# Kernel tuning notes

Measured on AMD Instinct MI355X. Metric: run time of the kernel, lower is better.

## Reference

```python
import jax, jax.numpy as jnp
import numpy as np

D_MODEL, N_HEADS, D_HEAD = 1024, 16, 64
B, T = 4, 2048


def setup_inputs() -> dict:
    key = jax.random.key(0)
    k1, k2, k3 = jax.random.split(key, 3)
    x = jax.random.normal(k1, (B, T, D_MODEL), dtype=jnp.float32)
    w_qkv = jax.random.normal(k2, (3 * N_HEADS * D_HEAD, D_MODEL), dtype=jnp.float32) * 0.02
    w_out = jax.random.normal(k3, (D_MODEL, N_HEADS * D_HEAD), dtype=jnp.float32) * 0.02
    return {"x": x, "w_qkv": w_qkv, "w_out": w_out}


def reference(x, w_qkv, w_out):
    Bx, Tx, Dx = x.shape
    scale = D_HEAD ** (-0.5)
    qkv = jnp.einsum('btd,ed->bte', x, w_qkv)  # [B,T,3*H*Dh]
    q, k, v = jnp.split(qkv, 3, axis=-1)
    def heads(t):  # [B,T,H*Dh] -> [B,H,T,Dh]
        return t.reshape(Bx, Tx, N_HEADS, D_HEAD).transpose(0, 2, 1, 3)
    q, k, v = heads(q), heads(k), heads(v)
    att = jnp.einsum('bhqd,bhkd->bhqk', q, k) * scale
    causal = jnp.tril(jnp.ones((Tx, Tx), dtype=bool))
    att = jnp.where(causal, att, -jnp.inf)
    att = jax.nn.softmax(att, axis=-1)
    y = jnp.einsum('bhqk,bhkd->bhqd', att, v)
    y = y.transpose(0, 2, 1, 3).reshape(Bx, Tx, N_HEADS * D_HEAD)
    return jnp.einsum('bte,de->btd', y, w_out)
```

## Files before the change

kernel.cpp:

```cpp
#include <hip/hip_runtime.h>
#include <hip/hip_bf16.h>

#define T_SEQ   2048
#define HEADS   16
#define DH      64
#define DMODEL  1024
#define EQKV    3072
#define BT_TOT  8192

typedef __attribute__((ext_vector_type(8)))  __bf16 bf16x8;
typedef __attribute__((ext_vector_type(4)))  float  f32x4;
typedef __attribute__((ext_vector_type(16))) float  f32x16;
typedef unsigned short ushort_t;
typedef unsigned int   uint_t;

__device__ __forceinline__ ushort_t f2bfu(float x) {
    union { float f; uint_t u; } c; c.f = x;
    uint_t u = c.u;
    uint_t r = (u + 0x7fffu + ((u >> 16) & 1u)) >> 16;
    return (ushort_t)r;
}

__device__ __forceinline__ uint_t cvtpk(float lo, float hi) {
    uint_t r;
    asm volatile("v_cvt_pk_bf16_f32 %0, %1, %2" : "=v"(r) : "v"(lo), "v"(hi));
    return r;
}

__device__ __forceinline__ void gload16(const ushort_t* g, ushort_t* l) {
    __builtin_amdgcn_global_load_lds(
        (const __attribute__((address_space(1))) void*)g,
        (__attribute__((address_space(3))) void*)l,
        16, 0, 0);
}

__global__ void cvt_f32_bf16(const float* __restrict__ in, ushort_t* __restrict__ out, int n4) {
    int i = blockIdx.x * blockDim.x + threadIdx.x;
    if (i >= n4) return;
    const float4 v = ((const float4*)in)[i];
    ushort_t r0 = f2bfu(v.x), r1 = f2bfu(v.y), r2 = f2bfu(v.z), r3 = f2bfu(v.w);
    uint_t lo = (uint_t)r0 | ((uint_t)r1 << 16);
    uint_t hi = (uint_t)r2 | ((uint_t)r3 << 16);
    ((uint2*)out)[i] = make_uint2(lo, hi);
}

#define BM 128
#define BN 128
#define BK 32

template<int MODE>
__global__ __launch_bounds__(256) void gemm_bt(const ushort_t* __restrict__ A,
                                               const ushort_t* __restrict__ Bt,
                                               void* __restrict__ Cv,
                                               ushort_t* __restrict__ VtOut,
                                               int M, int N, int K) {
    __shared__ __align__(16) ushort_t As[BM * BK];
    __shared__ __align__(16) ushort_t Bs[BN * BK];

    const int tid  = threadIdx.x;
    const int gx   = gridDim.x;
    int flat = blockIdx.y * gx + blockIdx.x;
    const int nwg  = gx * gridDim.y;
    flat = (flat & 7) * (nwg >> 3) + (flat >> 3);
    const int bn   = flat % gx, bm = flat / gx;
    const int row0 = bm * BM, col0 = bn * BN;
    const int wid  = tid >> 6, lane = tid & 63;
    const int wr   = wid >> 1, wc = wid & 1;
    const int lr   = lane & 15, lg = lane >> 4;

    const int lrow = lane >> 2;
    const int lcol = (lane & 3) * 8;

    f32x4 acc[4][4] = {};

    for (int k0 = 0; k0 < K; k0 += BK) {
        #pragma unroll
        for (int it = 0; it < 2; ++it) {
            const int c = wid * 2 + it;
            const int r = c * 16 + lrow;
            gload16(&A [(size_t)(row0 + r) * K + k0 + lcol], &As[c * 512]);
            gload16(&Bt[(size_t)(col0 + r) * K + k0 + lcol], &Bs[c * 512]);
        }
        __syncthreads();

        bf16x8 bfr[4];
        #pragma unroll
        for (int n = 0; n < 4; ++n)
            bfr[n] = *(const bf16x8*)&Bs[(wc * 64 + n * 16 + lr) * BK + lg * 8];
        #pragma unroll
        for (int m = 0; m < 4; ++m) {
            bf16x8 a = *(const bf16x8*)&As[(wr * 64 + m * 16 + lr) * BK + lg * 8];
            #pragma unroll
            for (int n = 0; n < 4; ++n)
                acc[m][n] = __builtin_amdgcn_mfma_f32_16x16x32_bf16(a, bfr[n], acc[m][n], 0, 0, 0);
        }
        __syncthreads();
    }

    if (MODE == 2 && col0 >= 2048) {
        #pragma unroll
        for (int m = 0; m < 4; ++m) {
            int rowb = row0 + wr * 64 + m * 16 + lg * 4;
            #pragma unroll
            for (int n = 0; n < 4; ++n) {
                int e = col0 - 2048 + wc * 64 + n * 16 + lr;
                uint_t lo = (uint_t)f2bfu(acc[m][n][0]) | ((uint_t)f2bfu(acc[m][n][1]) << 16);
                uint_t hi = (uint_t)f2bfu(acc[m][n][2]) | ((uint_t)f2bfu(acc[m][n][3]) << 16);
                *(uint2*)&VtOut[(size_t)e * BT_TOT + rowb] = make_uint2(lo, hi);
            }
        }
    } else {
        const int ostride = (MODE == 2) ? 2048 : N;
        #pragma unroll
        for (int m = 0; m < 4; ++m) {
            int rowb = row0 + wr * 64 + m * 16 + lg * 4;
            #pragma unroll
            for (int n = 0; n < 4; ++n) {
                int col = col0 + wc * 64 + n * 16 + lr;
                #pragma unroll
                for (int i = 0; i < 4; ++i) {
                    if (MODE == 2)
                        ((ushort_t*)Cv)[(size_t)(rowb + i) * ostride + col] = f2bfu(acc[m][n][i]);
                    else
                        ((float*)Cv)[(size_t)(rowb + i) * ostride + col] = acc[m][n][i];
                }
            }
        }
    }
}

__global__ __launch_bounds__(128, 2) void attn_fwd(const ushort_t* __restrict__ qk,
                                                   const ushort_t* __restrict__ vt,
                                                   ushort_t* __restrict__ y) {
    const int flat = blockIdx.x;
    const int xcd  = flat & 7;
    const int s    = flat >> 3;
    const int bh   = xcd * 8 + (s & 7);
    const int bx   = 31 - (s >> 3);
    const int b    = bh >> 4, h = bh & 15;
    const int tid  = threadIdx.x, lane = tid & 63;
    const int w    = tid >> 6;
    const int i    = lane & 31;
    const int hh   = lane >> 5;
    const int bT   = b * T_SEQ;

    __shared__ __align__(16) ushort_t KsL[2][64 * 64];
    __shared__ __align__(16) ushort_t VlL[2][64 * 64];

    const int q0 = bx * 64 + w * 32;
    const int qg = q0 + i;

    bf16x8 qf[4];
    {
        const ushort_t* qrow = qk + (size_t)(bT + qg) * 2048 + h * DH;
        #pragma unroll
        for (int kd = 0; kd < 4; ++kd) {
            bf16x8 q = *(const bf16x8*)&qrow[kd * 16 + hh * 8];
            #pragma unroll
            for (int j = 0; j < 8; ++j)
                ((ushort_t*)&q)[j] = f2bfu(__bfloat162float(
                    *(const __hip_bfloat16*)&((ushort_t*)&q)[j]) * 0.125f);
            qf[kd] = q;
        }
    }

    const int lr8    = lane >> 3;
    const int schunk = ((lane & 7) ^ lr8) * 8;
    const int rbase  = w * 32;

    float m = -1e30f, lsum = 0.f;
    f32x16 o0 = {}, o1 = {};

    const int nt = bx + 1;

    #pragma unroll
    for (int it = 0; it < 4; ++it) {
        const int rg = rbase + it * 8;
        const int r  = rg + lr8;
        gload16(&qk[(size_t)(bT + r) * 2048 + 1024 + h * DH + schunk], &KsL[0][rg * 64]);
        gload16(&vt[(size_t)(h * DH + r) * BT_TOT + bT + schunk],      &VlL[0][rg * 64]);
    }
    __syncthreads();

    for (int t = 0; t < nt; ++t) {
        const int cb = t & 1, nb = cb ^ 1;
        const bool has_next = (t + 1 < nt);
        const int kmin = t * 64;

        if (has_next) {
            const int kt = kmin + 64;
            #pragma unroll
            for (int it = 0; it < 4; ++it) {
                const int rg = rbase + it * 8;
                const int r  = rg + lr8;
                gload16(&qk[(size_t)(bT + kt + r) * 2048 + 1024 + h * DH + schunk], &KsL[nb][rg * 64]);
                gload16(&vt[(size_t)(h * DH + r) * BT_TOT + bT + kt + schunk],      &VlL[nb][rg * 64]);
            }
        }

        f32x16 st[2] = {};
        __builtin_amdgcn_s_setprio(1);
        #pragma unroll
        for (int kd = 0; kd < 4; ++kd) {
            const int cq = kd * 2 + hh;
            bf16x8 ka0 = *(const bf16x8*)&KsL[cb][i * 64        + ((cq ^ (i & 7)) * 8)];
            bf16x8 ka1 = *(const bf16x8*)&KsL[cb][(32 + i) * 64 + ((cq ^ (i & 7)) * 8)];
            st[0] = __builtin_amdgcn_mfma_f32_32x32x16_bf16(ka0, qf[kd], st[0], 0, 0, 0);
            st[1] = __builtin_amdgcn_mfma_f32_32x32x16_bf16(ka1, qf[kd], st[1], 0, 0, 0);
        }
        __builtin_amdgcn_s_setprio(0);

        const bool needmask = (kmin + 63) > q0;
        float pm = -1e30f;
        #pragma unroll
        for (int g = 0; g < 2; ++g) {
            #pragma unroll
            for (int r = 0; r < 16; ++r) {
                float v = st[g][r];
                if (needmask) {
                    int kv = kmin + g * 32 + (r & 3) + 8 * (r >> 2) + 4 * hh;
                    v = (kv <= qg) ? v : -1e30f;
                    st[g][r] = v;
                }
                pm = fmaxf(pm, v);
            }
        }
        pm = fmaxf(pm, __shfl_xor(pm, 32));

        if (!__all(pm - m <= 8.f)) {
            const float mnew = fmaxf(m, pm);
            const float corr = __expf(m - mnew);
            m = mnew;
            lsum *= corr;
            #pragma unroll
            for (int r = 0; r < 16; ++r) { o0[r] *= corr; o1[r] *= corr; }
        }
        float rs = 0.f;
        #pragma unroll
        for (int g = 0; g < 2; ++g) {
            #pragma unroll
            for (int r = 0; r < 16; ++r) {
                float p = __expf(st[g][r] - m);
                st[g][r] = p;
                rs += p;
            }
        }
        rs += __shfl_xor(rs, 32);
        lsum += rs;

        #pragma unroll
        for (int ks = 0; ks < 4; ++ks) {
            const int g = ks >> 1, b0 = (ks & 1) * 8;
            uint_t w0 = cvtpk(st[g][b0 + 0], st[g][b0 + 1]);
            uint_t w1 = cvtpk(st[g][b0 + 2], st[g][b0 + 3]);
            uint_t w2 = cvtpk(st[g][b0 + 4], st[g][b0 + 5]);
            uint_t w3 = cvtpk(st[g][b0 + 6], st[g][b0 + 7]);
            uint_t e0 = (uint_t)__shfl_xor((int)w0, 32);
            uint_t e1 = (uint_t)__shfl_xor((int)w1, 32);
            uint_t e2 = (uint_t)__shfl_xor((int)w2, 32);
            uint_t e3 = (uint_t)__shfl_xor((int)w3, 32);
            union { uint_t u[4]; bf16x8 v; } fr;
            fr.u[0] = hh ? e2 : w0;
            fr.u[1] = hh ? e3 : w1;
            fr.u[2] = hh ? w2 : e0;
            fr.u[3] = hh ? w3 : e1;
            const int ct = ks * 2 + hh;
            bf16x8 va0 = *(const bf16x8*)&VlL[cb][i * 64        + ((ct ^ (i & 7)) * 8)];
            bf16x8 va1 = *(const bf16x8*)&VlL[cb][(32 + i) * 64 + ((ct ^ (i & 7)) * 8)];
            __builtin_amdgcn_s_setprio(1);
            o0 = __builtin_amdgcn_mfma_f32_32x32x16_bf16(va0, fr.v, o0, 0, 0, 0);
            o1 = __builtin_amdgcn_mfma_f32_32x32x16_bf16(va1, fr.v, o1, 0, 0, 0);
            __builtin_amdgcn_s_setprio(0);
        }

        __syncthreads();
    }

    const float inv = 1.f / lsum;
    ushort_t* yrow = y + (size_t)(bT + qg) * (HEADS * DH) + h * DH;
    #pragma unroll
    for (int df = 0; df < 2; ++df) {
        const f32x16 oo = df ? o1 : o0;
        #pragma unroll
        for (int q4 = 0; q4 < 4; ++q4) {
            uint_t w0 = cvtpk(oo[q4 * 4 + 0] * inv, oo[q4 * 4 + 1] * inv);
            uint_t w1 = cvtpk(oo[q4 * 4 + 2] * inv, oo[q4 * 4 + 3] * inv);
            uint2 pk = make_uint2(w0, w1);
            *(uint2*)&yrow[df * 32 + q4 * 8 + hh * 4] = pk;
        }
    }
}

extern "C" void kernel_launch(void* const* d_in, const int* in_sizes, int n_in,
                              void* d_out, int out_size, void* d_ws, size_t ws_size,
                              hipStream_t stream) {
    const float* x     = (const float*)d_in[0];
    const float* w_qkv = (const float*)d_in[1];
    const float* w_out = (const float*)d_in[2];

    const int BT = BT_TOT;

    char* ws = (char*)d_ws;
    ushort_t* xb  = (ushort_t*)(ws);
    ushort_t* wqb = (ushort_t*)(ws + 16777216);
    ushort_t* wob = (ushort_t*)(ws + 23068672);
    ushort_t* qkb = (ushort_t*)(ws + 25165824);
    ushort_t* vtb = (ushort_t*)(ws + 58720256);
    ushort_t* yb  = (ushort_t*)(ws + 75497472);

    {
        int n4 = (BT * DMODEL) / 4;
        cvt_f32_bf16<<<(n4 + 255) / 256, 256, 0, stream>>>(x, xb, n4);
        n4 = (EQKV * DMODEL) / 4;
        cvt_f32_bf16<<<(n4 + 255) / 256, 256, 0, stream>>>(w_qkv, wqb, n4);
        n4 = (DMODEL * DMODEL) / 4;
        cvt_f32_bf16<<<(n4 + 255) / 256, 256, 0, stream>>>(w_out, wob, n4);
    }

    {
        dim3 grid(EQKV / BN, BT / BM);
        gemm_bt<2><<<grid, 256, 0, stream>>>(xb, wqb, (void*)qkb, vtb, BT, EQKV, DMODEL);
    }

    {
        attn_fwd<<<2048, 128, 0, stream>>>(qkb, vtb, yb);
    }

    {
        dim3 grid(DMODEL / BN, BT / BM);
        gemm_bt<0><<<grid, 256, 0, stream>>>(yb, wob, d_out, nullptr, BT, DMODEL, DMODEL);
    }
}
```

Baseline: 284.3 us.

## Use 128-query attention blocks with four waves, permlane swaps and exp2 softmax

Each attention block now covers 128 query rows with four waves (256 threads) that share one double-buffered K/V tile stream, which halves global K/V loads per query. Waves whose query range sits entirely before a key tile skip that tile's compute, though they still wait at the barrier. The cross-half reductions and the P-fragment exchange use permlane32_swap instead of ds shuffles. Softmax moves to base-2 by folding log2(e) into the Q scale and calling v_exp_f32 directly. In exchange, causal imbalance inside a block grows and the kernel asks for higher occupancy through launch bounds.

```diff
diff --git a/kernel.cpp b/kernel.cpp
--- a/kernel.cpp
+++ b/kernel.cpp
@@ -11,6 +11,7 @@
 typedef __attribute__((ext_vector_type(8)))  __bf16 bf16x8;
 typedef __attribute__((ext_vector_type(4)))  float  f32x4;
 typedef __attribute__((ext_vector_type(16))) float  f32x16;
+typedef unsigned int __attribute__((ext_vector_type(2))) uint2v;
 typedef unsigned short ushort_t;
 typedef unsigned int   uint_t;
 
@@ -24,6 +25,29 @@
 __device__ __forceinline__ uint_t cvtpk(float lo, float hi) {
     uint_t r;
     asm volatile("v_cvt_pk_bf16_f32 %0, %1, %2" : "=v"(r) : "v"(lo), "v"(hi));
+    return r;
+}
+
+__device__ __forceinline__ void plswap(uint_t& a, uint_t& b) {
+    uint2v r = __builtin_amdgcn_permlane32_swap(a, b, false, false);
+    a = r[0]; b = r[1];
+}
+
+__device__ __forceinline__ float halfmax(float x) {
+    uint_t a = __float_as_uint(x), b = a;
+    plswap(a, b);
+    return fmaxf(__uint_as_float(a), __uint_as_float(b));
+}
+
+__device__ __forceinline__ float halfadd(float x) {
+    uint_t a = __float_as_uint(x), b = a;
+    plswap(a, b);
+    return __uint_as_float(a) + __uint_as_float(b);
+}
+
+__device__ __forceinline__ float exp2v(float x) {
+    float r;
+    asm("v_exp_f32 %0, %1" : "=v"(r) : "v"(x));
     return r;
 }
 
@@ -129,17 +153,17 @@
     }
 }
 
-__global__ __launch_bounds__(128, 2) void attn_fwd(const ushort_t* __restrict__ qk,
+__global__ __launch_bounds__(256, 4) void attn_fwd(const ushort_t* __restrict__ qk,
                                                    const ushort_t* __restrict__ vt,
                                                    ushort_t* __restrict__ y) {
     const int flat = blockIdx.x;
     const int xcd  = flat & 7;
     const int s    = flat >> 3;
     const int bh   = xcd * 8 + (s & 7);
-    const int bx   = 31 - (s >> 3);
+    const int bx   = 15 - (s >> 3);
     const int b    = bh >> 4, h = bh & 15;
     const int tid  = threadIdx.x, lane = tid & 63;
-    const int w    = tid >> 6;
+    const int wid  = tid >> 6;
     const int i    = lane & 31;
     const int hh   = lane >> 5;
     const int bT   = b * T_SEQ;
@@ -147,11 +171,12 @@
     __shared__ __align__(16) ushort_t KsL[2][64 * 64];
     __shared__ __align__(16) ushort_t VlL[2][64 * 64];
 
-    const int q0 = bx * 64 + w * 32;
+    const int q0 = bx * 128 + wid * 32;
     const int qg = q0 + i;
 
     bf16x8 qf[4];
     {
+        const float qsc = 0.18033688011112042f;
         const ushort_t* qrow = qk + (size_t)(bT + qg) * 2048 + h * DH;
         #pragma unroll
         for (int kd = 0; kd < 4; ++kd) {
@@ -159,23 +184,22 @@
             #pragma unroll
             for (int j = 0; j < 8; ++j)
                 ((ushort_t*)&q)[j] = f2bfu(__bfloat162float(
-                    *(const __hip_bfloat16*)&((ushort_t*)&q)[j]) * 0.125f);
+                    *(const __hip_bfloat16*)&((ushort_t*)&q)[j]) * qsc);
             qf[kd] = q;
         }
     }
 
     const int lr8    = lane >> 3;
     const int schunk = ((lane & 7) ^ lr8) * 8;
-    const int rbase  = w * 32;
 
     float m = -1e30f, lsum = 0.f;
     f32x16 o0 = {}, o1 = {};
 
-    const int nt = bx + 1;
+    const int nt = 2 * bx + 2;
 
     #pragma unroll
-    for (int it = 0; it < 4; ++it) {
-        const int rg = rbase + it * 8;
+    for (int it = 0; it < 2; ++it) {
+        const int rg = wid * 16 + it * 8;
         const int r  = rg + lr8;
         gload16(&qk[(size_t)(bT + r) * 2048 + 1024 + h * DH + schunk], &KsL[0][rg * 64]);
         gload16(&vt[(size_t)(h * DH + r) * BT_TOT + bT + schunk],      &VlL[0][rg * 64]);
@@ -190,87 +214,83 @@
         if (has_next) {
             const int kt = kmin + 64;
             #pragma unroll
-            for (int it = 0; it < 4; ++it) {
-                const int rg = rbase + it * 8;
+            for (int it = 0; it < 2; ++it) {
+                const int rg = wid * 16 + it * 8;
                 const int r  = rg + lr8;
                 gload16(&qk[(size_t)(bT + kt + r) * 2048 + 1024 + h * DH + schunk], &KsL[nb][rg * 64]);
                 gload16(&vt[(size_t)(h * DH + r) * BT_TOT + bT + kt + schunk],      &VlL[nb][rg * 64]);
             }
         }
 
-        f32x16 st[2] = {};
-        __builtin_amdgcn_s_setprio(1);
-        #pragma unroll
-        for (int kd = 0; kd < 4; ++kd) {
-            const int cq = kd * 2 + hh;
-            bf16x8 ka0 = *(const bf16x8*)&KsL[cb][i * 64        + ((cq ^ (i & 7)) * 8)];
-            bf16x8 ka1 = *(const bf16x8*)&KsL[cb][(32 + i) * 64 + ((cq ^ (i & 7)) * 8)];
-            st[0] = __builtin_amdgcn_mfma_f32_32x32x16_bf16(ka0, qf[kd], st[0], 0, 0, 0);
-            st[1] = __builtin_amdgcn_mfma_f32_32x32x16_bf16(ka1, qf[kd], st[1], 0, 0, 0);
-        }
-        __builtin_amdgcn_s_setprio(0);
-
-        const bool needmask = (kmin + 63) > q0;
-        float pm = -1e30f;
-        #pragma unroll
-        for (int g = 0; g < 2; ++g) {
-            #pragma unroll
-            for (int r = 0; r < 16; ++r) {
-                float v = st[g][r];
-                if (needmask) {
-                    int kv = kmin + g * 32 + (r & 3) + 8 * (r >> 2) + 4 * hh;
-                    v = (kv <= qg) ? v : -1e30f;
-                    st[g][r] = v;
+        if (kmin <= q0 + 31) {
+            f32x16 st[2] = {};
+            __builtin_amdgcn_s_setprio(1);
+            #pragma unroll
+            for (int kd = 0; kd < 4; ++kd) {
+                const int cq = kd * 2 + hh;
+                bf16x8 ka0 = *(const bf16x8*)&KsL[cb][i * 64        + ((cq ^ (i & 7)) * 8)];
+                bf16x8 ka1 = *(const bf16x8*)&KsL[cb][(32 + i) * 64 + ((cq ^ (i & 7)) * 8)];
+                st[0] = __builtin_amdgcn_mfma_f32_32x32x16_bf16(ka0, qf[kd], st[0], 0, 0, 0);
+                st[1] = __builtin_amdgcn_mfma_f32_32x32x16_bf16(ka1, qf[kd], st[1], 0, 0, 0);
+            }
+            __builtin_amdgcn_s_setprio(0);
+
+            const bool needmask = (kmin + 63) > q0;
+            float pm = -1e30f;
+            #pragma unroll
+            for (int g = 0; g < 2; ++g) {
+                #pragma unroll
+                for (int r = 0; r < 16; ++r) {
+                    float v = st[g][r];
+                    if (needmask) {
+                        int kv = kmin + g * 32 + (r & 3) + 8 * (r >> 2) + 4 * hh;
+                        v = (kv <= qg) ? v : -1e30f;
+                        st[g][r] = v;
+                    }
+                    pm = fmaxf(pm, v);
                 }
-                pm = fmaxf(pm, v);
-            }
-        }
-        pm = fmaxf(pm, __shfl_xor(pm, 32));
-
-        if (!__all(pm - m <= 8.f)) {
-            const float mnew = fmaxf(m, pm);
-            const float corr = __expf(m - mnew);
-            m = mnew;
-            lsum *= corr;
-            #pragma unroll
-            for (int r = 0; r < 16; ++r) { o0[r] *= corr; o1[r] *= corr; }
-        }
-        float rs = 0.f;
-        #pragma unroll
-        for (int g = 0; g < 2; ++g) {
-            #pragma unroll
-            for (int r = 0; r < 16; ++r) {
-                float p = __expf(st[g][r] - m);
-                st[g][r] = p;
-                rs += p;
-            }
-        }
-        rs += __shfl_xor(rs, 32);
-        lsum += rs;
-
-        #pragma unroll
-        for (int ks = 0; ks < 4; ++ks) {
-            const int g = ks >> 1, b0 = (ks & 1) * 8;
-            uint_t w0 = cvtpk(st[g][b0 + 0], st[g][b0 + 1]);
-            uint_t w1 = cvtpk(st[g][b0 + 2], st[g][b0 + 3]);
-            uint_t w2 = cvtpk(st[g][b0 + 4], st[g][b0 + 5]);
-            uint_t w3 = cvtpk(st[g][b0 + 6], st[g][b0 + 7]);
-            uint_t e0 = (uint_t)__shfl_xor((int)w0, 32);
-            uint_t e1 = (uint_t)__shfl_xor((int)w1, 32);
-            uint_t e2 = (uint_t)__shfl_xor((int)w2, 32);
-            uint_t e3 = (uint_t)__shfl_xor((int)w3, 32);
-            union { uint_t u[4]; bf16x8 v; } fr;
-            fr.u[0] = hh ? e2 : w0;
-            fr.u[1] = hh ? e3 : w1;
-            fr.u[2] = hh ? w2 : e0;
-            fr.u[3] = hh ? w3 : e1;
-            const int ct = ks * 2 + hh;
-            bf16x8 va0 = *(const bf16x8*)&VlL[cb][i * 64        + ((ct ^ (i & 7)) * 8)];
-            bf16x8 va1 = *(const bf16x8*)&VlL[cb][(32 + i) * 64 + ((ct ^ (i & 7)) * 8)];
-            __builtin_amdgcn_s_setprio(1);
-            o0 = __builtin_amdgcn_mfma_f32_32x32x16_bf16(va0, fr.v, o0, 0, 0, 0);
-            o1 = __builtin_amdgcn_mfma_f32_32x32x16_bf16(va1, fr.v, o1, 0, 0, 0);
-            __builtin_amdgcn_s_setprio(0);
+            }
+            pm = halfmax(pm);
+
+            if (!__all(pm - m <= 11.5416f)) {
+                const float mnew = fmaxf(m, pm);
+                const float corr = exp2v(m - mnew);
+                m = mnew;
+                lsum *= corr;
+                #pragma unroll
+                for (int r = 0; r < 16; ++r) { o0[r] *= corr; o1[r] *= corr; }
+            }
+            float rs = 0.f;
+            #pragma unroll
+            for (int g = 0; g < 2; ++g) {
+                #pragma unroll
+                for (int r = 0; r < 16; ++r) {
+                    float p = exp2v(st[g][r] - m);
+                    st[g][r] = p;
+                    rs += p;
+                }
+            }
+            lsum += halfadd(rs);
+
+            #pragma unroll
+            for (int ks = 0; ks < 4; ++ks) {
+                const int g = ks >> 1, b0 = (ks & 1) * 8;
+                uint_t w0 = cvtpk(st[g][b0 + 0], st[g][b0 + 1]);
+                uint_t w1 = cvtpk(st[g][b0 + 2], st[g][b0 + 3]);
+                uint_t w2 = cvtpk(st[g][b0 + 4], st[g][b0 + 5]);
+                uint_t w3 = cvtpk(st[g][b0 + 6], st[g][b0 + 7]);
+                plswap(w0, w2);
+                plswap(w1, w3);
+                union { uint_t u[4]; bf16x8 v; } fr;
+                fr.u[0] = w0; fr.u[1] = w1; fr.u[2] = w2; fr.u[3] = w3;
+                const int ct = ks * 2 + hh;
+                bf16x8 va0 = *(const bf16x8*)&VlL[cb][i * 64        + ((ct ^ (i & 7)) * 8)];
+                bf16x8 va1 = *(const bf16x8*)&VlL[cb][(32 + i) * 64 + ((ct ^ (i & 7)) * 8)];
+                __builtin_amdgcn_s_setprio(1);
+                o0 = __builtin_amdgcn_mfma_f32_32x32x16_bf16(va0, fr.v, o0, 0, 0, 0);
+                o1 = __builtin_amdgcn_mfma_f32_32x32x16_bf16(va1, fr.v, o1, 0, 0, 0);
+                __builtin_amdgcn_s_setprio(0);
+            }
         }
 
         __syncthreads();
@@ -323,7 +343,7 @@
     }
 
     {
-        attn_fwd<<<2048, 128, 0, stream>>>(qkb, vtb, yb);
+        attn_fwd<<<1024, 256, 0, stream>>>(qkb, vtb, yb);
     }
 
     {
```

Result: no change. 282.6 us (-0.6%).
